# Kernel tuning notes

Hardware: AMD Instinct MI355X
Metric: run time of the kernel (lower is better)

The kernel has to match this reference:

```python
import jax, jax.numpy as jnp
import numpy as np

THRESHOLD = 0.05

def binarize101(w, threshold):
    # Ternary quantization to {-1, 0, +1}: zero inside the dead-zone [-thr, thr].
    pos = (w > threshold).astype(w.dtype)
    neg = (w < -threshold).astype(w.dtype)
    return pos - neg

def setup_inputs() -> dict:
    key = jax.random.key(0)
    k1, k2, k3 = jax.random.split(key, 3)
    x = jax.random.normal(k1, (8192, 4096), dtype=jnp.float32)
    weight = jax.random.normal(k2, (4096, 4096), dtype=jnp.float32)
    bias = jax.random.normal(k3, (4096,), dtype=jnp.float32)
    return {"x": x, "weight": weight, "bias": bias}

def reference(x, weight, bias):
    wb = binarize101(weight, THRESHOLD)
    # F.linear: x @ wb.T + bias ; x: [N, in], weight: [out, in] -> [N, out]
    return jnp.einsum('ni,oi->no', x, wb) + bias
```

## Files before the change

kernel.cpp:

```cpp
#include <hip/hip_runtime.h>

typedef float floatx16 __attribute__((ext_vector_type(16)));
typedef __bf16 bf16x8 __attribute__((ext_vector_type(8)));
using u16 = unsigned short;
using u32 = unsigned int;

#define GLOBAL_AS __attribute__((address_space(1)))
#define LDS_AS    __attribute__((address_space(3)))

__device__ __forceinline__ u32 rne_bf16(float f) {
  u32 u = __float_as_uint(f);
  return (u + 0x7FFFu + ((u >> 16) & 1u)) >> 16;
}

__global__ __launch_bounds__(256) void cvt_x_perm(const float* __restrict__ x,
                                                  u16* __restrict__ xb, int K) {
  __shared__ u16 sm[16384];
  const int tid = threadIdx.x;
  const int Kt = K >> 6;
  const int pn = blockIdx.x / Kt, tt = blockIdx.x % Kt;
  const float* src = x + (size_t)pn * 256 * K + tt * 64;
#pragma unroll
  for (int j = 0; j < 16; ++j) {
    const int fc = j * 256 + tid;
    const int row = fc >> 4, kl4 = fc & 15;
    const float4 v = *(const float4*)(src + (size_t)row * K + kl4 * 4);
    uint2 o;
    o.x = rne_bf16(v.x) | (rne_bf16(v.y) << 16);
    o.y = rne_bf16(v.z) | (rne_bf16(v.w) << 16);
    const int gi = row >> 5, rowin = row & 31;
    const int ks = kl4 >> 2;
    const int lane = rowin + 32 * ((kl4 >> 1) & 1);
    const int e4 = (kl4 & 1) * 4;
    *(uint2*)(sm + gi * 2048 + ks * 512 + lane * 8 + e4) = o;
  }
  __syncthreads();
  u16* dst = xb + (size_t)pn * 256 * K + (size_t)tt * 16384;
#pragma unroll
  for (int j = 0; j < 8; ++j) {
    const int o = (j * 256 + tid) * 8;
    *(uint4*)(dst + o) = *(const uint4*)(sm + o);
  }
}

__global__ __launch_bounds__(256) void quant_w_perm(const float* __restrict__ w,
                                                    u16* __restrict__ wb, int K) {
  __shared__ u16 sm[16384];
  const int tid = threadIdx.x;
  const int Kt = K >> 6;
  const int pn = blockIdx.x / Kt, tt = blockIdx.x % Kt;
  const float* src = w + (size_t)pn * 256 * K + tt * 64;
#pragma unroll
  for (int j = 0; j < 16; ++j) {
    const int fc = j * 256 + tid;
    const int row = fc >> 4, kl4 = fc & 15;
    const float4 v = *(const float4*)(src + (size_t)row * K + kl4 * 4);
    float vv[4] = {v.x, v.y, v.z, v.w};
    u32 r[4];
#pragma unroll
    for (int e = 0; e < 4; ++e)
      r[e] = (vv[e] > 0.05f) ? 0x3F80u : ((vv[e] < -0.05f) ? 0xBF80u : 0u);
    uint2 o;
    o.x = r[0] | (r[1] << 16);
    o.y = r[2] | (r[3] << 16);
    const int gi = row >> 5, rowin = row & 31;
    const int ks = kl4 >> 2;
    const int lane = rowin + 32 * ((kl4 >> 1) & 1);
    const int e4 = (kl4 & 1) * 4;
    *(uint2*)(sm + gi * 2048 + ks * 512 + lane * 8 + e4) = o;
  }
  __syncthreads();
  u16* dst = wb + (size_t)pn * 256 * K + (size_t)tt * 16384;
#pragma unroll
  for (int j = 0; j < 8; ++j) {
    const int o = (j * 256 + tid) * 8;
    *(uint4*)(dst + o) = *(const uint4*)(sm + o);
  }
}

__global__ __launch_bounds__(512, 2) void gemm_bin_3232(
    const u16* __restrict__ Ap, const u16* __restrict__ Bp,
    const float* __restrict__ bias, float* __restrict__ C,
    int M, int N, int K) {
  __shared__ u16 lds[65536];

  const int tid = threadIdx.x;
  const int w = tid >> 6, l = tid & 63;
  const int wr = w >> 2, wc = w & 3;

  const int nbn = N >> 8;
  int wg = blockIdx.x;
  const int nwg = gridDim.x;
  if ((nwg & 7) == 0) wg = (wg & 7) * (nwg >> 3) + (wg >> 3);
  const int bm = wg / nbn, bn = wg % nbn;

  const int T = K >> 6;

  const u16* const Abase = Ap + (size_t)bm * ((size_t)K << 8) + tid * 8;
  const u16* const Bbase = Bp + (size_t)bn * ((size_t)K << 8) + tid * 8;

  const u16* const afp0 = lds + wr * 8192 + l * 8;
  const u16* const bfp0 = lds + 16384 + wc * 4096 + l * 8;

  floatx16 acc[4][2] = {};
  bf16x8 af[8], bflo[4], bfhi[4];

#define GLOAD(gptr, u16off)                                                    \
  __builtin_amdgcn_global_load_lds((const GLOBAL_AS void*)(gptr),              \
                                   (LDS_AS void*)(lds + (u16off)), 16, 0, 0)
#define BARRIER __builtin_amdgcn_s_barrier()
#define LGKM0  do { asm volatile("s_waitcnt lgkmcnt(0)" ::: "memory");         \
                    __builtin_amdgcn_sched_barrier(0); } while (0)

  GLOAD(Abase + 0 * 4096,      0 + tid * 8);
  GLOAD(Abase + 2 * 4096,   8192 + tid * 8);
  GLOAD(Bbase + 0 * 4096,  16384 + tid * 8);
  GLOAD(Bbase + 1 * 4096,  20480 + tid * 8);
  GLOAD(Bbase + 2 * 4096,  24576 + tid * 8);
  GLOAD(Bbase + 3 * 4096,  28672 + tid * 8);
  GLOAD(Abase + 1 * 4096,   4096 + tid * 8);
  GLOAD(Abase + 3 * 4096,  12288 + tid * 8);
  asm volatile("s_waitcnt vmcnt(2)" ::: "memory");
  BARRIER;

  for (int t = 0; t < T; ++t) {
    const int bufc = (t & 1) << 15;
    const int bufn = bufc ^ 32768;
    const bool doSt = (t + 1 < T);
    const size_t tn = (size_t)(t + 1) * 16384;

    const u16* afp = afp0 + bufc;
    const u16* bfp = bfp0 + bufc;

#pragma unroll
    for (int m = 0; m < 2; ++m)
#pragma unroll
      for (int ks = 0; ks < 4; ++ks)
        af[m * 4 + ks] = *(const bf16x8*)(afp + m * 2048 + ks * 512);
#pragma unroll
    for (int ks = 0; ks < 4; ++ks) bflo[ks] = *(const bf16x8*)(bfp + ks * 512);
    if (doSt) {
      GLOAD(Abase + tn + 0 * 4096, bufn + 0 + tid * 8);
      GLOAD(Abase + tn + 2 * 4096, bufn + 8192 + tid * 8);
    }
    asm volatile("s_waitcnt lgkmcnt(8)" ::: "memory");
    BARRIER;
    LGKM0;
    __builtin_amdgcn_s_setprio(1);
#pragma unroll
    for (int ks = 0; ks < 4; ++ks)
#pragma unroll
      for (int m = 0; m < 2; ++m)
        acc[m][0] = __builtin_amdgcn_mfma_f32_32x32x16_bf16(
            af[m * 4 + ks], bflo[ks], acc[m][0], 0, 0, 0);
    __builtin_amdgcn_s_setprio(0);
    if (doSt) asm volatile("s_waitcnt vmcnt(4)" ::: "memory");
    else      asm volatile("s_waitcnt vmcnt(2)" ::: "memory");
    BARRIER;

#pragma unroll
    for (int ks = 0; ks < 4; ++ks) bfhi[ks] = *(const bf16x8*)(bfp + 2048 + ks * 512);
    if (doSt) {
      GLOAD(Bbase + tn + 0 * 4096, bufn + 16384 + tid * 8);
      GLOAD(Bbase + tn + 1 * 4096, bufn + 20480 + tid * 8);
    }
    BARRIER;
    LGKM0;
    __builtin_amdgcn_s_setprio(1);
#pragma unroll
    for (int ks = 0; ks < 4; ++ks)
#pragma unroll
      for (int m = 0; m < 2; ++m)
        acc[m][1] = __builtin_amdgcn_mfma_f32_32x32x16_bf16(
            af[m * 4 + ks], bfhi[ks], acc[m][1], 0, 0, 0);
    __builtin_amdgcn_s_setprio(0);
    if (doSt) asm volatile("s_waitcnt vmcnt(4)" ::: "memory");
    else      asm volatile("s_waitcnt vmcnt(0)" ::: "memory");
    BARRIER;

#pragma unroll
    for (int m = 0; m < 2; ++m)
#pragma unroll
      for (int ks = 0; ks < 4; ++ks)
        af[m * 4 + ks] = *(const bf16x8*)(afp + 4096 + m * 2048 + ks * 512);
    if (doSt) {
      GLOAD(Bbase + tn + 2 * 4096, bufn + 24576 + tid * 8);
      GLOAD(Bbase + tn + 3 * 4096, bufn + 28672 + tid * 8);
    }
    asm volatile("s_waitcnt lgkmcnt(4)" ::: "memory");
    BARRIER;
    LGKM0;
    __builtin_amdgcn_s_setprio(1);
#pragma unroll
    for (int ks = 0; ks < 4; ++ks)
#pragma unroll
      for (int m = 0; m < 2; ++m)
        acc[2 + m][0] = __builtin_amdgcn_mfma_f32_32x32x16_bf16(
            af[m * 4 + ks], bflo[ks], acc[2 + m][0], 0, 0, 0);
    __builtin_amdgcn_s_setprio(0);
    if (doSt) asm volatile("s_waitcnt vmcnt(4)" ::: "memory");
    BARRIER;

    if (doSt) {
      GLOAD(Abase + tn + 1 * 4096, bufn + 4096 + tid * 8);
      GLOAD(Abase + tn + 3 * 4096, bufn + 12288 + tid * 8);
    }
    BARRIER;
    __builtin_amdgcn_s_setprio(1);
#pragma unroll
    for (int ks = 0; ks < 4; ++ks)
#pragma unroll
      for (int m = 0; m < 2; ++m)
        acc[2 + m][1] = __builtin_amdgcn_mfma_f32_32x32x16_bf16(
            af[m * 4 + ks], bfhi[ks], acc[2 + m][1], 0, 0, 0);
    __builtin_amdgcn_s_setprio(0);
    if (doSt) asm volatile("s_waitcnt vmcnt(2)" ::: "memory");
    BARRIER;
  }
#undef GLOAD
#undef BARRIER
#undef LGKM0

  const int colq = l & 31;
  const int hi4 = (l >> 5) * 4;
#pragma unroll
  for (int m = 0; m < 4; ++m) {
    const int rowb = bm * 256 + wr * 128 + m * 32 + hi4;
#pragma unroll
    for (int n = 0; n < 2; ++n) {
      const int col = bn * 256 + wc * 64 + n * 32 + colq;
      const float bv = bias[col];
      float* cp = C + (size_t)rowb * N + col;
#pragma unroll
      for (int q = 0; q < 16; ++q) {
        const int dr = (q & 3) + 8 * (q >> 2);
        cp[(size_t)dr * N] = acc[m][n][q] + bv;
      }
    }
  }
}

__global__ void gemm_naive_kernel(const float* __restrict__ x, const float* __restrict__ wgt,
                                  const float* __restrict__ bias, float* __restrict__ out,
                                  int M, int N, int K) {
  long long idx = (long long)blockIdx.x * blockDim.x + threadIdx.x;
  if (idx >= (long long)M * N) return;
  int o = (int)(idx % N);
  int m = (int)(idx / N);
  const float* xr = x + (size_t)m * K;
  const float* wr = wgt + (size_t)o * K;
  float s = 0.f;
  for (int i = 0; i < K; ++i) {
    float wv = wr[i];
    float t = (wv > 0.05f) ? 1.f : ((wv < -0.05f) ? -1.f : 0.f);
    s = fmaf(xr[i], t, s);
  }
  out[idx] = s + bias[o];
}

extern "C" void kernel_launch(void* const* d_in, const int* in_sizes, int n_in,
                              void* d_out, int out_size, void* d_ws, size_t ws_size,
                              hipStream_t stream) {
  const float* x    = (const float*)d_in[0];
  const float* wgt  = (const float*)d_in[1];
  const float* bias = (const float*)d_in[2];
  float* out = (float*)d_out;

  const int N = in_sizes[2];
  const int K = in_sizes[1] / N;
  const int M = in_sizes[0] / K;

  const size_t need = ((size_t)M * K + (size_t)N * K) * sizeof(u16);
  if (ws_size >= need && (M % 256 == 0) && (N % 256 == 0) && (K % 64 == 0) && K >= 128) {
    u16* xb = (u16*)d_ws;
    u16* wb = xb + (size_t)M * K;
    const int Kt = K / 64;
    cvt_x_perm<<<(M / 256) * Kt, 256, 0, stream>>>(x, xb, K);
    quant_w_perm<<<(N / 256) * Kt, 256, 0, stream>>>(wgt, wb, K);
    const int grid = (M / 256) * (N / 256);
    gemm_bin_3232<<<grid, 512, 0, stream>>>(xb, wb, bias, out, M, N, K);
  } else {
    const long long total = (long long)M * N;
    gemm_naive_kernel<<<(unsigned)((total + 255) / 256), 256, 0, stream>>>(x, wgt, bias, out, M, N, K);
  }
}
```

Baseline: 297.0 us.

## Deepen GEMM global-to-LDS prefetch to two K-tiles ahead

Restructures the double-buffered GEMM main loop so global-to-LDS loads are issued for tile t+2 into the current buffer as soon as each part of it is consumed. The remaining A half for t+1 goes to the other buffer, and the per-phase vmcnt waits are replaced by a single wait at the end of each iteration. The goal is more load latency in flight and fewer wait stalls between MFMA phases. The cost is tighter buffer-reuse ordering, which leans on barriers to avoid overwriting LDS still being read, and the fast path now requires K >= 192.

```diff
diff --git a/kernel.cpp b/kernel.cpp
--- a/kernel.cpp
+++ b/kernel.cpp
@@ -78,7 +78,7 @@
   }
 }
 
-__global__ __launch_bounds__(512, 2) void gemm_bin_3232(
+__global__ __launch_bounds__(512, 2) void gemm_bin_m201d(
     const u16* __restrict__ Ap, const u16* __restrict__ Bp,
     const float* __restrict__ bias, float* __restrict__ C,
     int M, int N, int K) {
@@ -120,14 +120,26 @@
   GLOAD(Bbase + 3 * 4096,  28672 + tid * 8);
   GLOAD(Abase + 1 * 4096,   4096 + tid * 8);
   GLOAD(Abase + 3 * 4096,  12288 + tid * 8);
-  asm volatile("s_waitcnt vmcnt(2)" ::: "memory");
+  if (T > 1) {
+    GLOAD(Abase + 16384 + 0 * 4096, 32768 + 0 + tid * 8);
+    GLOAD(Abase + 16384 + 2 * 4096, 32768 + 8192 + tid * 8);
+    GLOAD(Bbase + 16384 + 0 * 4096, 32768 + 16384 + tid * 8);
+    GLOAD(Bbase + 16384 + 1 * 4096, 32768 + 20480 + tid * 8);
+    GLOAD(Bbase + 16384 + 2 * 4096, 32768 + 24576 + tid * 8);
+    GLOAD(Bbase + 16384 + 3 * 4096, 32768 + 28672 + tid * 8);
+    asm volatile("s_waitcnt vmcnt(6)" ::: "memory");
+  } else {
+    asm volatile("s_waitcnt vmcnt(0)" ::: "memory");
+  }
   BARRIER;
 
   for (int t = 0; t < T; ++t) {
     const int bufc = (t & 1) << 15;
-    const int bufn = bufc ^ 32768;
-    const bool doSt = (t + 1 < T);
-    const size_t tn = (size_t)(t + 1) * 16384;
+    const int bufo = bufc ^ 32768;
+    const bool st1 = (t + 1 < T);
+    const bool st2 = (t + 2 < T);
+    const size_t tn1 = (size_t)(t + 1) * 16384;
+    const size_t tn2 = (size_t)(t + 2) * 16384;
 
     const u16* afp = afp0 + bufc;
     const u16* bfp = bfp0 + bufc;
@@ -139,9 +151,9 @@
         af[m * 4 + ks] = *(const bf16x8*)(afp + m * 2048 + ks * 512);
 #pragma unroll
     for (int ks = 0; ks < 4; ++ks) bflo[ks] = *(const bf16x8*)(bfp + ks * 512);
-    if (doSt) {
-      GLOAD(Abase + tn + 0 * 4096, bufn + 0 + tid * 8);
-      GLOAD(Abase + tn + 2 * 4096, bufn + 8192 + tid * 8);
+    if (st1) {
+      GLOAD(Abase + tn1 + 1 * 4096, bufo + 4096 + tid * 8);
+      GLOAD(Abase + tn1 + 3 * 4096, bufo + 12288 + tid * 8);
     }
     asm volatile("s_waitcnt lgkmcnt(8)" ::: "memory");
     BARRIER;
@@ -154,15 +166,13 @@
         acc[m][0] = __builtin_amdgcn_mfma_f32_32x32x16_bf16(
             af[m * 4 + ks], bflo[ks], acc[m][0], 0, 0, 0);
     __builtin_amdgcn_s_setprio(0);
-    if (doSt) asm volatile("s_waitcnt vmcnt(4)" ::: "memory");
-    else      asm volatile("s_waitcnt vmcnt(2)" ::: "memory");
     BARRIER;
 
 #pragma unroll
     for (int ks = 0; ks < 4; ++ks) bfhi[ks] = *(const bf16x8*)(bfp + 2048 + ks * 512);
-    if (doSt) {
-      GLOAD(Bbase + tn + 0 * 4096, bufn + 16384 + tid * 8);
-      GLOAD(Bbase + tn + 1 * 4096, bufn + 20480 + tid * 8);
+    if (st2) {
+      GLOAD(Abase + tn2 + 0 * 4096, bufc + 0 + tid * 8);
+      GLOAD(Abase + tn2 + 2 * 4096, bufc + 8192 + tid * 8);
     }
     BARRIER;
     LGKM0;
@@ -174,8 +184,6 @@
         acc[m][1] = __builtin_amdgcn_mfma_f32_32x32x16_bf16(
             af[m * 4 + ks], bfhi[ks], acc[m][1], 0, 0, 0);
     __builtin_amdgcn_s_setprio(0);
-    if (doSt) asm volatile("s_waitcnt vmcnt(4)" ::: "memory");
-    else      asm volatile("s_waitcnt vmcnt(0)" ::: "memory");
     BARRIER;
 
 #pragma unroll
@@ -183,9 +191,9 @@
 #pragma unroll
       for (int ks = 0; ks < 4; ++ks)
         af[m * 4 + ks] = *(const bf16x8*)(afp + 4096 + m * 2048 + ks * 512);
-    if (doSt) {
-      GLOAD(Bbase + tn + 2 * 4096, bufn + 24576 + tid * 8);
-      GLOAD(Bbase + tn + 3 * 4096, bufn + 28672 + tid * 8);
+    if (st2) {
+      GLOAD(Bbase + tn2 + 0 * 4096, bufc + 16384 + tid * 8);
+      GLOAD(Bbase + tn2 + 1 * 4096, bufc + 20480 + tid * 8);
     }
     asm volatile("s_waitcnt lgkmcnt(4)" ::: "memory");
     BARRIER;
@@ -198,12 +206,11 @@
         acc[2 + m][0] = __builtin_amdgcn_mfma_f32_32x32x16_bf16(
             af[m * 4 + ks], bflo[ks], acc[2 + m][0], 0, 0, 0);
     __builtin_amdgcn_s_setprio(0);
-    if (doSt) asm volatile("s_waitcnt vmcnt(4)" ::: "memory");
-    BARRIER;
-
-    if (doSt) {
-      GLOAD(Abase + tn + 1 * 4096, bufn + 4096 + tid * 8);
-      GLOAD(Abase + tn + 3 * 4096, bufn + 12288 + tid * 8);
+    BARRIER;
+
+    if (st2) {
+      GLOAD(Bbase + tn2 + 2 * 4096, bufc + 24576 + tid * 8);
+      GLOAD(Bbase + tn2 + 3 * 4096, bufc + 28672 + tid * 8);
     }
     BARRIER;
     __builtin_amdgcn_s_setprio(1);
@@ -214,7 +221,8 @@
         acc[2 + m][1] = __builtin_amdgcn_mfma_f32_32x32x16_bf16(
             af[m * 4 + ks], bfhi[ks], acc[2 + m][1], 0, 0, 0);
     __builtin_amdgcn_s_setprio(0);
-    if (doSt) asm volatile("s_waitcnt vmcnt(2)" ::: "memory");
+    if (st2) asm volatile("s_waitcnt vmcnt(6)" ::: "memory");
+    else     asm volatile("s_waitcnt vmcnt(0)" ::: "memory");
     BARRIER;
   }
 #undef GLOAD
@@ -271,14 +279,14 @@
   const int M = in_sizes[0] / K;
 
   const size_t need = ((size_t)M * K + (size_t)N * K) * sizeof(u16);
-  if (ws_size >= need && (M % 256 == 0) && (N % 256 == 0) && (K % 64 == 0) && K >= 128) {
+  if (ws_size >= need && (M % 256 == 0) && (N % 256 == 0) && (K % 64 == 0) && K >= 192) {
     u16* xb = (u16*)d_ws;
     u16* wb = xb + (size_t)M * K;
     const int Kt = K / 64;
     cvt_x_perm<<<(M / 256) * Kt, 256, 0, stream>>>(x, xb, K);
     quant_w_perm<<<(N / 256) * Kt, 256, 0, stream>>>(wgt, wb, K);
     const int grid = (M / 256) * (N / 256);
-    gemm_bin_3232<<<grid, 512, 0, stream>>>(xb, wb, bias, out, M, N, K);
+    gemm_bin_m201d<<<grid, 512, 0, stream>>>(xb, wb, bias, out, M, N, K);
   } else {
     const long long total = (long long)M * N;
     gemm_naive_kernel<<<(unsigned)((total + 255) / 256), 256, 0, stream>>>(x, wgt, bias, out, M, N, K);
```

After: 286.4 us (median of 2 runs). -3.6%, faster.
